# Kernel optimization log

Measured on AMD Instinct MI355X. Metric: run time of the kernel, lower is better.

The kernel has to match this reference:

```python
import jax, jax.numpy as jnp
import numpy as np

N = 8192
F_IN, F1, F2 = 11, 16, 32
HEADS = 3
D_CAT = 2 * F2          # 64, concat of interface + neighborhood branches
D_POOL = D_CAT * HEADS  # 192


def setup_inputs() -> dict:
    key = jax.random.key(0)
    ks = jax.random.split(key, 16)
    s = 0.1
    return {
        "x_int": jax.random.normal(ks[0], (N, F_IN), jnp.float32),
        "x_nh": jax.random.normal(ks[1], (N, F_IN), jnp.float32),
        # dense soft adjacencies, scaled ~1/N so aggregates stay O(1)
        "adj_int": jax.random.uniform(ks[2], (N, N), jnp.float32) / N,
        "adj_nh": jax.random.uniform(ks[3], (N, N), jnp.float32) / N,
        "W1_int": jax.random.normal(ks[4], (F_IN, F1), jnp.float32) * s,
        "b1_int": jnp.zeros((F1,), jnp.float32),
        "W1_nh": jax.random.normal(ks[5], (F_IN, F1), jnp.float32) * s,
        "b1_nh": jnp.zeros((F1,), jnp.float32),
        "W2_int": jax.random.normal(ks[6], (F1, F2), jnp.float32) * s,
        "b2_int": jnp.zeros((F2,), jnp.float32),
        "W2_nh": jax.random.normal(ks[7], (F1, F2), jnp.float32) * s,
        "b2_nh": jnp.zeros((F2,), jnp.float32),
        "W_att": jax.random.normal(ks[8], (D_CAT, HEADS), jnp.float32) * s,
        "W_dense": jax.random.normal(ks[9], (D_POOL, 1), jnp.float32) * s,
        "b_dense": jnp.zeros((1,), jnp.float32),
    }


def _dgcn(A, x, W, b):
    # diffusion graph conv: aggregate neighbors then linear + relu
    return jax.nn.relu(A @ (x @ W) + b)


def reference(x_int, x_nh, adj_int, adj_nh,
              W1_int, b1_int, W1_nh, b1_nh,
              W2_int, b2_int, W2_nh, b2_nh,
              W_att, W_dense, b_dense):
    # conv1 / conv2, two parallel graph branches
    h_int = _dgcn(adj_int, x_int, W1_int, b1_int)   # [N, 16]
    h_nh = _dgcn(adj_nh, x_nh, W1_nh, b1_nh)        # [N, 16]
    h_int = _dgcn(adj_int, h_int, W2_int, b2_int)   # [N, 32]
    h_nh = _dgcn(adj_nh, h_nh, W2_nh, b2_nh)        # [N, 32]
    h = jnp.concatenate([h_int, h_nh], axis=1)      # [N, 64]
    # multi-head tanh self-attention pooling over nodes
    scores = jnp.tanh(h @ W_att)                    # [N, heads]
    att = jax.nn.softmax(scores, axis=0)            # softmax over nodes
    pooled = jnp.einsum('nh,nd->hd', att, h).reshape(1, D_POOL)  # [1, 192]
    out = pooled @ W_dense + b_dense                # [1, 1]
    return jnp.squeeze(out, 1)                      # [1]
```

## Files before the change

kernel.cpp:

```cpp
#include <hip/hip_runtime.h>


constexpr int N = 8192;

#define GLOBAL_AS __attribute__((address_space(1)))
#define LDS_AS __attribute__((address_space(3)))

__device__ __forceinline__ void gload_lds16(const float* g, float* l) {
    __builtin_amdgcn_global_load_lds((const GLOBAL_AS void*)g, (LDS_AS void*)l, 16, 0, 0);
}

__global__ void k_dense_in(const float* __restrict__ x0, const float* __restrict__ x1,
                           const float* __restrict__ W0, const float* __restrict__ W1,
                           float* __restrict__ o0, float* __restrict__ o1) {
    const int branch = blockIdx.y;
    const float* __restrict__ x = branch ? x1 : x0;
    const float* __restrict__ W = branch ? W1 : W0;
    float* __restrict__ o = branch ? o1 : o0;
    __shared__ float sW[11 * 16];
    if (threadIdx.x < 176) sW[threadIdx.x] = W[threadIdx.x];
    __syncthreads();
    const int n = blockIdx.x * blockDim.x + threadIdx.x;
    float xr[11];
#pragma unroll
    for (int j = 0; j < 11; ++j) xr[j] = x[n * 11 + j];
    float acc[16];
#pragma unroll
    for (int f = 0; f < 16; ++f) acc[f] = 0.f;
#pragma unroll
    for (int j = 0; j < 11; ++j)
#pragma unroll
        for (int f = 0; f < 16; ++f) acc[f] += xr[j] * sW[j * 16 + f];
#pragma unroll
    for (int q = 0; q < 4; ++q) {
        float4 r = make_float4(acc[q * 4 + 0], acc[q * 4 + 1], acc[q * 4 + 2], acc[q * 4 + 3]);
        *reinterpret_cast<float4*>(&o[n * 16 + q * 4]) = r;
    }
}

__global__ void k_dense_mid(const float* __restrict__ h0, const float* __restrict__ h1,
                            const float* __restrict__ W0, const float* __restrict__ W1,
                            float* __restrict__ o0, float* __restrict__ o1) {
    const int branch = blockIdx.y;
    const float* __restrict__ h = branch ? h1 : h0;
    const float* __restrict__ W = branch ? W1 : W0;
    float* __restrict__ o = branch ? o1 : o0;
    __shared__ float sW[16 * 32];
    for (int i = threadIdx.x; i < 512; i += blockDim.x) sW[i] = W[i];
    __syncthreads();
    const int n = blockIdx.x * blockDim.x + threadIdx.x;
    float hr[16];
#pragma unroll
    for (int q = 0; q < 4; ++q)
        *reinterpret_cast<float4*>(&hr[q * 4]) =
            *reinterpret_cast<const float4*>(&h[n * 16 + q * 4]);
    float acc[32];
#pragma unroll
    for (int f = 0; f < 32; ++f) acc[f] = 0.f;
#pragma unroll
    for (int j = 0; j < 16; ++j)
#pragma unroll
        for (int f = 0; f < 32; ++f) acc[f] += hr[j] * sW[j * 32 + f];
#pragma unroll
    for (int q = 0; q < 8; ++q) {
        float4 r = make_float4(acc[q * 4 + 0], acc[q * 4 + 1], acc[q * 4 + 2], acc[q * 4 + 3]);
        *reinterpret_cast<float4*>(&o[n * 32 + q * 4]) = r;
    }
}

template <int F>
__global__ __launch_bounds__(256, 2) void k_spmm(
    const float* __restrict__ A0, const float* __restrict__ A1,
    const float* __restrict__ Pm0, const float* __restrict__ Pm1,
    const float* __restrict__ b0, const float* __restrict__ b1,
    float* __restrict__ o0, float* __restrict__ o1, int ostride) {
    constexpr int TN = F / 4;
    constexpr int PJ = TN / 4;
    constexpr int KT = 256;
    constexpr int NT = N / KT;
    const int branch = blockIdx.y;
    const float* __restrict__ A = branch ? A1 : A0;
    const float* __restrict__ Pm = branch ? Pm1 : Pm0;
    const float* __restrict__ bias = branch ? b1 : b0;
    float* __restrict__ o = branch ? o1 : o0;

    __shared__ float tile[2][32 * KT];

    const int lane = threadIdx.x & 63;
    const int wave = threadIdx.x >> 6;
    const int kg = lane & 15;
    const int cg = lane >> 4;
    const int c0 = cg * TN;
    const int row0 = blockIdx.x * 32;
    const float* gsrc = A + (size_t)(row0 + wave * 8) * N + lane * 4;

    auto stage = [&](int buf, int K0) {
#pragma unroll
        for (int r = 0; r < 8; ++r)
            gload_lds16(gsrc + (size_t)r * N + K0, &tile[buf][(wave * 8 + r) * KT]);
    };

    float acc[8][TN];
#pragma unroll
    for (int m = 0; m < 8; ++m)
#pragma unroll
        for (int j = 0; j < TN; ++j) acc[m][j] = 0.f;

    stage(0, 0);

    for (int it = 0; it < NT; ++it) {
        const int K0 = it * KT;
        const int buf = it & 1;
        asm volatile("s_waitcnt vmcnt(0)" ::: "memory");
        __builtin_amdgcn_sched_barrier(0);
        float4 p[4][4][PJ];
#pragma unroll
        for (int ks = 0; ks < 4; ++ks)
#pragma unroll
            for (int t = 0; t < 4; ++t)
#pragma unroll
                for (int j = 0; j < PJ; ++j)
                    p[ks][t][j] = *reinterpret_cast<const float4*>(
                        Pm + (size_t)(K0 + ks * 64 + kg * 4 + t) * F + c0 + j * 4);
        __builtin_amdgcn_sched_barrier(0);
        if (it + 1 < NT) stage(buf ^ 1, K0 + KT);
        __builtin_amdgcn_sched_barrier(0);
#pragma unroll
        for (int ks = 0; ks < 4; ++ks) {
            const int kk = ks * 64 + kg * 4;
#pragma unroll
            for (int m = 0; m < 8; ++m) {
                const float4 a = *reinterpret_cast<const float4*>(
                    &tile[buf][(wave * 8 + m) * KT + kk]);
#pragma unroll
                for (int t = 0; t < 4; ++t) {
                    const float av = (t == 0) ? a.x : (t == 1) ? a.y : (t == 2) ? a.z : a.w;
#pragma unroll
                    for (int j = 0; j < PJ; ++j) {
                        acc[m][j * 4 + 0] += av * p[ks][t][j].x;
                        acc[m][j * 4 + 1] += av * p[ks][t][j].y;
                        acc[m][j * 4 + 2] += av * p[ks][t][j].z;
                        acc[m][j * 4 + 3] += av * p[ks][t][j].w;
                    }
                }
            }
        }
    }

#pragma unroll
    for (int m = 0; m < 8; ++m)
#pragma unroll
        for (int j = 0; j < TN; ++j) {
            float v = acc[m][j];
            v += __shfl_xor(v, 1);
            v += __shfl_xor(v, 2);
            v += __shfl_xor(v, 4);
            v += __shfl_xor(v, 8);
            acc[m][j] = v;
        }
    if (kg == 0) {
#pragma unroll
        for (int m = 0; m < 8; ++m)
#pragma unroll
            for (int j = 0; j < PJ; ++j) {
                float4 r;
                r.x = fmaxf(acc[m][j * 4 + 0] + bias[c0 + j * 4 + 0], 0.f);
                r.y = fmaxf(acc[m][j * 4 + 1] + bias[c0 + j * 4 + 1], 0.f);
                r.z = fmaxf(acc[m][j * 4 + 2] + bias[c0 + j * 4 + 2], 0.f);
                r.w = fmaxf(acc[m][j * 4 + 3] + bias[c0 + j * 4 + 3], 0.f);
                *reinterpret_cast<float4*>(
                    &o[(size_t)(row0 + wave * 8 + m) * ostride + c0 + j * 4]) = r;
            }
    }
}

__global__ void k_att_pool(const float* __restrict__ h, const float* __restrict__ Watt,
                           const float* __restrict__ Wd, float* __restrict__ partials) {
    __shared__ float sWa[64 * 3];
    __shared__ float sWd[192];
    for (int i = threadIdx.x; i < 192; i += blockDim.x) {
        sWa[i] = Watt[i];
        sWd[i] = Wd[i];
    }
    __syncthreads();
    const int n = blockIdx.x * blockDim.x + threadIdx.x;
    float hv[64];
#pragma unroll
    for (int q = 0; q < 16; ++q)
        *reinterpret_cast<float4*>(&hv[q * 4]) =
            *reinterpret_cast<const float4*>(&h[(size_t)n * 64 + q * 4]);
    float s0 = 0.f, s1 = 0.f, s2 = 0.f;
#pragma unroll
    for (int d = 0; d < 64; ++d) {
        s0 += hv[d] * sWa[d * 3 + 0];
        s1 += hv[d] * sWa[d * 3 + 1];
        s2 += hv[d] * sWa[d * 3 + 2];
    }
    float dot0 = 0.f, dot1 = 0.f, dot2 = 0.f;
#pragma unroll
    for (int d = 0; d < 64; ++d) {
        dot0 += hv[d] * sWd[0 * 64 + d];
        dot1 += hv[d] * sWd[1 * 64 + d];
        dot2 += hv[d] * sWd[2 * 64 + d];
    }
    const float e0 = expf(tanhf(s0));
    const float e1 = expf(tanhf(s1));
    const float e2 = expf(tanhf(s2));
    float vals[6] = {e0, e1, e2, e0 * dot0, e1 * dot1, e2 * dot2};
#pragma unroll
    for (int i = 0; i < 6; ++i) {
        float v = vals[i];
#pragma unroll
        for (int off = 1; off < 64; off <<= 1) v += __shfl_xor(v, off);
        vals[i] = v;
    }
    __shared__ float sred[4][6];
    const int wave = threadIdx.x >> 6, lane = threadIdx.x & 63;
    if (lane == 0) {
#pragma unroll
        for (int i = 0; i < 6; ++i) sred[wave][i] = vals[i];
    }
    __syncthreads();
    if (threadIdx.x == 0) {
#pragma unroll
        for (int i = 0; i < 6; ++i)
            partials[blockIdx.x * 6 + i] = sred[0][i] + sred[1][i] + sred[2][i] + sred[3][i];
    }
}

__global__ void k_att_final(const float* __restrict__ partials, const float* __restrict__ bd,
                            float* __restrict__ out) {
    if (threadIdx.x == 0) {
        float Z0 = 0.f, Z1 = 0.f, Z2 = 0.f, U0 = 0.f, U1 = 0.f, U2 = 0.f;
        for (int b = 0; b < 32; ++b) {
            Z0 += partials[b * 6 + 0];
            Z1 += partials[b * 6 + 1];
            Z2 += partials[b * 6 + 2];
            U0 += partials[b * 6 + 3];
            U1 += partials[b * 6 + 4];
            U2 += partials[b * 6 + 5];
        }
        out[0] = U0 / Z0 + U1 / Z1 + U2 / Z2 + bd[0];
    }
}

extern "C" void kernel_launch(void* const* d_in, const int* in_sizes, int n_in,
                              void* d_out, int out_size, void* d_ws, size_t ws_size,
                              hipStream_t stream) {
    const float* x_int   = (const float*)d_in[0];
    const float* x_nh    = (const float*)d_in[1];
    const float* adj_int = (const float*)d_in[2];
    const float* adj_nh  = (const float*)d_in[3];
    const float* W1_int  = (const float*)d_in[4];
    const float* b1_int  = (const float*)d_in[5];
    const float* W1_nh   = (const float*)d_in[6];
    const float* b1_nh   = (const float*)d_in[7];
    const float* W2_int  = (const float*)d_in[8];
    const float* b2_int  = (const float*)d_in[9];
    const float* W2_nh   = (const float*)d_in[10];
    const float* b2_nh   = (const float*)d_in[11];
    const float* W_att   = (const float*)d_in[12];
    const float* W_dense = (const float*)d_in[13];
    const float* b_dense = (const float*)d_in[14];

    float* ws = (float*)d_ws;
    float* P1_0 = ws;
    float* P1_1 = ws + 131072;
    float* H1_0 = ws + 262144;
    float* H1_1 = ws + 393216;
    float* P2_0 = ws + 524288;
    float* P2_1 = ws + 786432;
    float* hcat = ws + 1048576;
    float* partials = ws + 1572864;
    float* out = (float*)d_out;

    k_dense_in<<<dim3(32, 2), 256, 0, stream>>>(x_int, x_nh, W1_int, W1_nh, P1_0, P1_1);
    k_spmm<16><<<dim3(256, 2), 256, 0, stream>>>(adj_int, adj_nh, P1_0, P1_1,
                                                 b1_int, b1_nh, H1_0, H1_1, 16);
    k_dense_mid<<<dim3(32, 2), 256, 0, stream>>>(H1_0, H1_1, W2_int, W2_nh, P2_0, P2_1);
    k_spmm<32><<<dim3(256, 2), 256, 0, stream>>>(adj_int, adj_nh, P2_0, P2_1,
                                                 b2_int, b2_nh, hcat, hcat + 32, 64);
    k_att_pool<<<32, 256, 0, stream>>>(hcat, W_att, W_dense, partials);
    k_att_final<<<1, 64, 0, stream>>>(partials, b_dense, out);
}
```

Measured before the change: 527.9 us.

## Template SpMM K-tile size, use smaller tile for F=32, stagger K start per wave

Makes the K tile size a template parameter and uses a 128-wide tile for the 32-feature aggregation pass, reducing the per-iteration register footprint of the P operand buffer. It also rotates the starting K tile per block and wave so concurrent waves read different parts of the P matrix and adjacency rows, aiming to reduce cache/channel contention. Smaller tiles mean more loop iterations and more sync overhead per byte loaded.

```diff
diff --git a/kernel.cpp b/kernel.cpp
--- a/kernel.cpp
+++ b/kernel.cpp
@@ -68,7 +68,7 @@
     }
 }
 
-template <int F>
+template <int F, int KT>
 __global__ __launch_bounds__(256, 2) void k_spmm(
     const float* __restrict__ A0, const float* __restrict__ A1,
     const float* __restrict__ Pm0, const float* __restrict__ Pm1,
@@ -76,8 +76,8 @@
     float* __restrict__ o0, float* __restrict__ o1, int ostride) {
     constexpr int TN = F / 4;
     constexpr int PJ = TN / 4;
-    constexpr int KT = 256;
     constexpr int NT = N / KT;
+    constexpr int KS = KT / 64;
     const int branch = blockIdx.y;
     const float* __restrict__ A = branch ? A1 : A0;
     const float* __restrict__ Pm = branch ? Pm1 : Pm0;
@@ -92,12 +92,26 @@
     const int cg = lane >> 4;
     const int c0 = cg * TN;
     const int row0 = blockIdx.x * 32;
-    const float* gsrc = A + (size_t)(row0 + wave * 8) * N + lane * 4;
+    const int phase = (blockIdx.x * 4 + wave) & (NT - 1);
+
+    const float* gsrc;
+    if constexpr (KT == 256) {
+        gsrc = A + (size_t)(row0 + wave * 8) * N + lane * 4;
+    } else {
+        gsrc = A + (size_t)(row0 + wave * 8 + (lane >> 5)) * N + (lane & 31) * 4;
+    }
 
     auto stage = [&](int buf, int K0) {
-#pragma unroll
-        for (int r = 0; r < 8; ++r)
-            gload_lds16(gsrc + (size_t)r * N + K0, &tile[buf][(wave * 8 + r) * KT]);
+        if constexpr (KT == 256) {
+#pragma unroll
+            for (int r = 0; r < 8; ++r)
+                gload_lds16(gsrc + (size_t)r * N + K0, &tile[buf][(wave * 8 + r) * KT]);
+        } else {
+#pragma unroll
+            for (int i = 0; i < 4; ++i)
+                gload_lds16(gsrc + (size_t)(2 * i) * N + K0,
+                            &tile[buf][(wave * 8 + 2 * i) * KT]);
+        }
     };
 
     float acc[8][TN];
@@ -106,16 +120,16 @@
 #pragma unroll
         for (int j = 0; j < TN; ++j) acc[m][j] = 0.f;
 
-    stage(0, 0);
+    stage(0, phase * KT);
 
     for (int it = 0; it < NT; ++it) {
-        const int K0 = it * KT;
+        const int K0 = ((it + phase) & (NT - 1)) * KT;
         const int buf = it & 1;
         asm volatile("s_waitcnt vmcnt(0)" ::: "memory");
         __builtin_amdgcn_sched_barrier(0);
-        float4 p[4][4][PJ];
-#pragma unroll
-        for (int ks = 0; ks < 4; ++ks)
+        float4 p[KS][4][PJ];
+#pragma unroll
+        for (int ks = 0; ks < KS; ++ks)
 #pragma unroll
             for (int t = 0; t < 4; ++t)
 #pragma unroll
@@ -123,10 +137,10 @@
                     p[ks][t][j] = *reinterpret_cast<const float4*>(
                         Pm + (size_t)(K0 + ks * 64 + kg * 4 + t) * F + c0 + j * 4);
         __builtin_amdgcn_sched_barrier(0);
-        if (it + 1 < NT) stage(buf ^ 1, K0 + KT);
+        if (it + 1 < NT) stage(buf ^ 1, ((it + 1 + phase) & (NT - 1)) * KT);
         __builtin_amdgcn_sched_barrier(0);
 #pragma unroll
-        for (int ks = 0; ks < 4; ++ks) {
+        for (int ks = 0; ks < KS; ++ks) {
             const int kk = ks * 64 + kg * 4;
 #pragma unroll
             for (int m = 0; m < 8; ++m) {
@@ -275,11 +289,11 @@
     float* out = (float*)d_out;
 
     k_dense_in<<<dim3(32, 2), 256, 0, stream>>>(x_int, x_nh, W1_int, W1_nh, P1_0, P1_1);
-    k_spmm<16><<<dim3(256, 2), 256, 0, stream>>>(adj_int, adj_nh, P1_0, P1_1,
-                                                 b1_int, b1_nh, H1_0, H1_1, 16);
+    k_spmm<16, 256><<<dim3(256, 2), 256, 0, stream>>>(adj_int, adj_nh, P1_0, P1_1,
+                                                      b1_int, b1_nh, H1_0, H1_1, 16);
     k_dense_mid<<<dim3(32, 2), 256, 0, stream>>>(H1_0, H1_1, W2_int, W2_nh, P2_0, P2_1);
-    k_spmm<32><<<dim3(256, 2), 256, 0, stream>>>(adj_int, adj_nh, P2_0, P2_1,
-                                                 b2_int, b2_nh, hcat, hcat + 32, 64);
+    k_spmm<32, 128><<<dim3(256, 2), 256, 0, stream>>>(adj_int, adj_nh, P2_0, P2_1,
+                                                      b2_int, b2_nh, hcat, hcat + 32, 64);
     k_att_pool<<<32, 256, 0, stream>>>(hcat, W_att, W_dense, partials);
     k_att_final<<<1, 64, 0, stream>>>(partials, b_dense, out);
 }
```

New measurement: 506.1 us. -4.1%, faster.
